# Kernel optimization log

Measured on AMD Instinct MI355X. Metric: run time of the kernel, lower is better.

## Reference

```python
import jax, jax.numpy as jnp
import numpy as np

B, TT, TS, H, O = 16, 512, 512, 1024, 1024


def setup_inputs() -> dict:
    key = jax.random.key(0)
    k1, k2, k3, k4, k5 = jax.random.split(key, 5)
    ht = jax.random.normal(k1, (B, TT, H), dtype=jnp.float32)
    hs = jax.random.normal(k2, (B, TS, H), dtype=jnp.float32)
    source = jax.random.randint(k3, (B, TS), 0, 10000, dtype=jnp.int32)
    # glorot-like scaling for weights
    W_a = jax.random.normal(k4, (H, H), dtype=jnp.float32) * (2.0 / (H + H)) ** 0.5
    W_c = jax.random.normal(k5, (2 * H, O), dtype=jnp.float32) * (2.0 / (2 * H + O)) ** 0.5
    b = jnp.zeros((O,), dtype=jnp.float32)
    return {"ht": ht, "hs": hs, "source": source, "W_a": W_a, "W_c": W_c, "b": b}


def reference(ht, hs, source, W_a, W_c, b):
    # score = ht . (hs @ W_a)^T : [B, Tt, Ts]
    keys = jnp.einsum('bsk,kl->bsl', hs, W_a)
    score = jnp.einsum('btk,bsk->bts', ht, keys)
    # stable exp with max subtraction (matches original manual softmax)
    score = jnp.exp(score - jnp.max(score, axis=-1, keepdims=True))
    # sequence mask from count of non-pad (non-zero) source tokens
    lens = jnp.sum((source != 0).astype(jnp.int32), axis=1)          # [B]
    mask = (jnp.arange(TS)[None, :] < lens[:, None]).astype(score.dtype)  # [B, Ts]
    score = score * mask[:, None, :]
    a = score / jnp.sum(score, axis=-1, keepdims=True)               # [B, Tt, Ts]
    c = jnp.einsum('bts,bsk->btk', a, hs)                            # context [B, Tt, H]
    h = jnp.concatenate([c, ht], axis=-1)                            # [B, Tt, 2H]
    return jnp.tanh(jnp.einsum('btk,kl->btl', h, W_c) + b)
```

## Files before the change

kernel.cpp:

```cpp
#include <hip/hip_runtime.h>
#include <math.h>

typedef unsigned short u16;
typedef unsigned int u32;

using f32x4 = __attribute__((ext_vector_type(4))) float;
using s16x8 = __attribute__((ext_vector_type(8))) short;
using f16x8 = __attribute__((ext_vector_type(8))) _Float16;
using u32x4 = __attribute__((ext_vector_type(4))) u32;

#define DEVI static __device__ __forceinline__

#define BB 16
#define TT 512
#define TS 512
#define HH 1024
#define OO 1024

DEVI void split_bf(float x, u16& hb, u16& lb) {
    u32 xb = __float_as_uint(x);
    float hf = __uint_as_float(xb & 0xffff0000u);
    hb = (u16)(xb >> 16);
    lb = (u16)(__float_as_uint(x - hf) >> 16);
}

DEVI float ub(u16 h) { return __uint_as_float((u32)h << 16); }

template <int PREC> struct FragT;
template <> struct FragT<0> { using T = s16x8; };
template <> struct FragT<1> { using T = f16x8; };

DEVI f32x4 mfma16(s16x8 a, s16x8 b, f32x4 c) {
    return __builtin_amdgcn_mfma_f32_16x16x32_bf16(a, b, c, 0, 0, 0);
}
DEVI f32x4 mfma16(f16x8 a, f16x8 b, f32x4 c) {
    return __builtin_amdgcn_mfma_f32_16x16x32_f16(a, b, c, 0, 0, 0);
}

DEVI void gl16(const void* g, void* l) {
    __builtin_amdgcn_global_load_lds(
        (__attribute__((address_space(1))) const void*)g,
        (__attribute__((address_space(3))) void*)l, 16, 0, 0);
}

__global__ void lens_kernel(const int* __restrict__ src, int* __restrict__ lens) {
    int b = blockIdx.x;
    int v = (src[b * TS + (int)threadIdx.x] != 0) ? 1 : 0;
    unsigned long long m = __ballot(v);
    __shared__ int part[8];
    if ((threadIdx.x & 63) == 0) part[threadIdx.x >> 6] = __popcll(m);
    __syncthreads();
    if (threadIdx.x == 0) {
        int s = 0;
#pragma unroll
        for (int i = 0; i < 8; ++i) s += part[i];
        lens[b] = s;
    }
}

template <int PREC>
__global__ void transpose_split_kernel(const float* __restrict__ src,
                                       u16* __restrict__ dhi, u16* __restrict__ dlo,
                                       int R, int C) {
    __shared__ float tile[32][33];
    long boff = (long)blockIdx.z * R * C;
    src += boff;
    dhi += boff;
    if (PREC == 0) dlo += boff;
    int c0 = blockIdx.x * 32, r0 = blockIdx.y * 32;
    int tx = threadIdx.x, ty = threadIdx.y;
#pragma unroll
    for (int i = 0; i < 32; i += 8)
        tile[ty + i][tx] = src[(long)(r0 + ty + i) * C + (c0 + tx)];
    __syncthreads();
#pragma unroll
    for (int i = 0; i < 32; i += 8) {
        float v = tile[tx][ty + i];
        long o = (long)(c0 + ty + i) * R + (r0 + tx);
        if constexpr (PREC == 0) {
            u16 hb, lb;
            split_bf(v, hb, lb);
            dhi[o] = hb;
            dlo[o] = lb;
        } else {
            dhi[o] = __builtin_bit_cast(u16, (_Float16)v);
        }
    }
}

__global__ void hs_prep_kernel(const float* __restrict__ src,
                               u16* __restrict__ rhi, u16* __restrict__ rlo,
                               u16* __restrict__ thi) {
    __shared__ float tile[32][33];
    long boff = (long)blockIdx.z * TS * HH;
    src += boff;
    rhi += boff;
    rlo += boff;
    thi += boff;
    int c0 = blockIdx.x * 32, r0 = blockIdx.y * 32;
    int tx = threadIdx.x, ty = threadIdx.y;
#pragma unroll
    for (int i = 0; i < 32; i += 8) {
        long o = (long)(r0 + ty + i) * HH + (c0 + tx);
        float v = src[o];
        tile[ty + i][tx] = v;
        u16 hb, lb;
        split_bf(v, hb, lb);
        rhi[o] = hb;
        rlo[o] = lb;
    }
    __syncthreads();
#pragma unroll
    for (int i = 0; i < 32; i += 8) {
        long o = (long)(c0 + ty + i) * TS + (r0 + tx);
        thi[o] = __builtin_bit_cast(u16, (_Float16)tile[tx][ty + i]);
    }
}

__global__ void htf_prep_kernel(const float* __restrict__ ht, u16* __restrict__ f) {
    long i = ((long)blockIdx.x * 256 + threadIdx.x) * 8;
    float4 v0 = *(const float4*)(ht + i);
    float4 v1 = *(const float4*)(ht + i + 4);
    float fv[8] = {v0.x, v0.y, v0.z, v0.w, v1.x, v1.y, v1.z, v1.w};
    f16x8 o;
#pragma unroll
    for (int j = 0; j < 8; ++j) o[j] = (_Float16)fv[j];
    *(f16x8*)(f + i) = o;
}

__global__ void softmax_mask_kernel(u16* __restrict__ h0, u16* __restrict__ l0,
                                    const u16* __restrict__ h1, const u16* __restrict__ l1,
                                    const int* __restrict__ lens) {
    long row = blockIdx.x;
    int len = lens[blockIdx.x >> 9];
    int lane = threadIdx.x;
    long o = row * TS + 8 * lane;
    s16x8 vh0 = *(const s16x8*)(h0 + o);
    s16x8 vl0 = *(const s16x8*)(l0 + o);
    s16x8 vh1 = *(const s16x8*)(h1 + o);
    s16x8 vl1 = *(const s16x8*)(l1 + o);
    float f[8];
#pragma unroll
    for (int i = 0; i < 8; ++i)
        f[i] = (ub((u16)vh0[i]) + ub((u16)vl0[i])) + (ub((u16)vh1[i]) + ub((u16)vl1[i]));
    float m = f[0];
#pragma unroll
    for (int i = 1; i < 8; ++i) m = fmaxf(m, f[i]);
#pragma unroll
    for (int os = 32; os > 0; os >>= 1) m = fmaxf(m, __shfl_xor(m, os));
    float e[8];
    float sum = 0.f;
#pragma unroll
    for (int i = 0; i < 8; ++i) {
        e[i] = (8 * lane + i < len) ? expf(f[i] - m) : 0.f;
        sum += e[i];
    }
#pragma unroll
    for (int os = 32; os > 0; os >>= 1) sum += __shfl_xor(sum, os);
    float inv = 1.0f / sum;
    f16x8 p;
#pragma unroll
    for (int i = 0; i < 8; ++i) p[i] = (_Float16)(e[i] * inv);
    *(f16x8*)(h0 + o) = p;
}

template <int PREC, int TERMS, int EPI, int ACON, int KSPLIT, int SWZ>
__global__ __launch_bounds__(512, 2)
void gemm_p(const u16* __restrict__ Ahi, const u16* __restrict__ Alo,
            const u16* __restrict__ A2,
            const u16* __restrict__ Bhi, const u16* __restrict__ Blo,
            float* __restrict__ C, u16* __restrict__ Chi, u16* __restrict__ Clo,
            const float* __restrict__ bias,
            int N, int K, int lda, int ldb,
            long sA, long sB, long sC, long sKh) {
    constexpr int SUBS = (TERMS == 3) ? 1 : 2;
    constexpr int BKI = 32 * SUBS;
    constexpr int SUBU = (TERMS == 3) ? 24576 : 12288;
    constexpr int BUFU = 24576;
    constexpr int AHo = 0;
    constexpr int ALof = 8192;
    constexpr int BHo = (TERMS == 3) ? 16384 : 8192;
    constexpr int BLof = 20480;

    __shared__ u16 lds[3 * BUFU];

    int bx, by, bz = 0;
    if (SWZ) {
        int id = blockIdx.x;
        int ns = ((id & 7) << 5) | (id >> 3);
        by = ns >> 3;
        bx = ns & 7;
    } else {
        bx = blockIdx.x;
        by = blockIdx.y;
        bz = blockIdx.z;
    }
    int kh = 0;
    if (KSPLIT == 2) {
        kh = bz & 1;
        bz >>= 1;
    }
    if (!ACON) {
        Ahi += (long)bz * sA + (long)kh * K;
        if (TERMS == 3) Alo += (long)bz * sA + (long)kh * K;
    }
    Bhi += (long)bz * sB + (long)kh * K;
    if (TERMS == 3) Blo += (long)bz * sB + (long)kh * K;

    int tid = threadIdx.x;
    int lane = tid & 63;
    int wave = tid >> 6;
    int wm = (wave >> 1) * 64;
    int wn = (wave & 1) * 64;
    int fr = lane & 15;
    int kq = lane >> 4;
    int m0 = by * 256;
    int n0 = bx * 128;

    f32x4 acc[4][4];
#pragma unroll
    for (int i = 0; i < 4; ++i)
#pragma unroll
        for (int j = 0; j < 4; ++j) acc[i][j] = (f32x4){0.f, 0.f, 0.f, 0.f};

    auto stage_arr = [&](int dst, const u16* g, int r0, int ldg, int k0, int cnt) {
#pragma unroll
        for (int h = 0; h < cnt; ++h) {
            int vt = tid + h * 512;
            int row = vt >> 2;
            int ls = (vt & 3) ^ ((row >> 1) & 3);
            const u16* gp = g + (long)(r0 + row) * ldg + (k0 + 8 * ls);
            u16* lp = lds + dst + ((tid & ~63) + h * 512) * 8;
            gl16(gp, lp);
        }
    };
    auto stage = [&](int bi, int t) {
#pragma unroll
        for (int s = 0; s < SUBS; ++s) {
            int ks = t * BKI + s * 32;
            int sb = bi * BUFU + s * ((TERMS == 3) ? 0 : SUBU);
            if (ACON) {
                if (ks < HH)
                    stage_arr(sb + AHo, Ahi, m0, lda, ks, 2);
                else
                    stage_arr(sb + AHo, A2, m0, lda, ks - HH, 2);
            } else {
                stage_arr(sb + AHo, Ahi, m0, lda, ks, 2);
                if (TERMS == 3) stage_arr(sb + ALof, Alo, m0, lda, ks, 2);
            }
            stage_arr(sb + BHo, Bhi, n0, ldb, ks, 1);
            if (TERMS == 3) stage_arr(sb + BLof, Blo, n0, ldb, ks, 1);
        }
    };

    const int NTI = K / BKI;
    stage(0, 0);
    stage(1, 1);
    stage(2, 2);
    asm volatile("s_waitcnt vmcnt(12)" ::: "memory");
    __builtin_amdgcn_sched_barrier(0);
    __builtin_amdgcn_s_barrier();
    __builtin_amdgcn_sched_barrier(0);

    using FT = typename FragT<PREC>::T;
    for (int t = 0; t < NTI; ++t) {
        if (t >= 1 && t + 2 < NTI) stage((t + 2) % 3, t + 2);

        const u16* Lb = lds + (t % 3) * BUFU;
#pragma unroll
        for (int s = 0; s < SUBS; ++s) {
            const u16* Ls = Lb + s * SUBU;
            FT afh[4], afl[4], bfh[4], bfl[4];
#pragma unroll
            for (int i = 0; i < 4; ++i) {
                int ra = wm + i * 16 + fr;
                int rb = wn + i * 16 + fr;
                int oa = ra * 32 + ((kq ^ ((ra >> 1) & 3)) << 3);
                int ob = rb * 32 + ((kq ^ ((rb >> 1) & 3)) << 3);
                afh[i] = *(const FT*)(Ls + AHo + oa);
                bfh[i] = *(const FT*)(Ls + BHo + ob);
                if (TERMS == 3) {
                    afl[i] = *(const FT*)(Ls + ALof + oa);
                    bfl[i] = *(const FT*)(Ls + BLof + ob);
                }
            }
            __builtin_amdgcn_s_setprio(1);
#pragma unroll
            for (int i = 0; i < 4; ++i)
#pragma unroll
                for (int j = 0; j < 4; ++j) {
                    acc[i][j] = mfma16(afh[i], bfh[j], acc[i][j]);
                    if (TERMS == 3) {
                        acc[i][j] = mfma16(afl[i], bfh[j], acc[i][j]);
                        acc[i][j] = mfma16(afh[i], bfl[j], acc[i][j]);
                    }
                }
            __builtin_amdgcn_s_setprio(0);
        }
        if (t < NTI - 1) {
            __builtin_amdgcn_sched_barrier(0);
            if (t + 2 < NTI)
                asm volatile("s_waitcnt vmcnt(6)" ::: "memory");
            else
                asm volatile("s_waitcnt vmcnt(0)" ::: "memory");
            __builtin_amdgcn_sched_barrier(0);
            __builtin_amdgcn_s_barrier();
            __builtin_amdgcn_sched_barrier(0);
        }
    }

    long obase = (long)bz * sC + (long)kh * sKh;
    int fq = (lane >> 4) * 4;
#pragma unroll
    for (int i = 0; i < 4; ++i)
#pragma unroll
        for (int j = 0; j < 4; ++j)
#pragma unroll
            for (int g = 0; g < 4; ++g) {
                int row = m0 + wm + i * 16 + fq + g;
                int col = n0 + wn + j * 16 + fr;
                long idx = obase + (long)row * N + col;
                float v = acc[i][j][g];
                if constexpr (EPI == 1) {
                    u16 h2, l2;
                    split_bf(v, h2, l2);
                    Chi[idx] = h2;
                    Clo[idx] = l2;
                } else if constexpr (EPI == 2) {
                    float x = v + bias[col];
                    float t2 = __expf(2.f * x);
                    C[idx] = 1.f - 2.f * __builtin_amdgcn_rcpf(t2 + 1.f);
                } else {
                    Chi[idx] = __builtin_bit_cast(u16, (_Float16)v);
                }
            }
}

template <int PREC, int ASRC, int EPI, int TERMS, int KSPLIT, bool SWZ>
__global__ __launch_bounds__(256, 2)
void gemm_u(const u16* __restrict__ Ahi, const u16* __restrict__ Alo,
            const float* __restrict__ Af,
            const u16* __restrict__ Bhi, const u16* __restrict__ Blo,
            float* __restrict__ C, u16* __restrict__ Chi, u16* __restrict__ Clo,
            const float* __restrict__ bias,
            int M, int N, int K, int lda, int ldb,
            long sA, long sB, long sC, long sKh) {
    int bx, by, bz;
    if (SWZ) {
        int id = blockIdx.x;
        int ns = ((id & 7) << 6) | (id >> 3);
        bx = ns & 7;
        by = ns >> 3;
        bz = 0;
    } else {
        bx = blockIdx.x;
        by = blockIdx.y;
        bz = blockIdx.z;
    }
    int kh = 0;
    if (KSPLIT == 2) {
        kh = bz & 1;
        bz >>= 1;
    }
    if (ASRC == 0) {
        Ahi += (long)bz * sA + (long)kh * K;
        if (TERMS == 3) Alo += (long)bz * sA + (long)kh * K;
    } else if (ASRC == 1) {
        Af += (long)bz * sA + (long)kh * K;
    }
    Bhi += (long)bz * sB + (long)kh * K;
    if (TERMS == 3) Blo += (long)bz * sB + (long)kh * K;

    int n0 = bx * 128;
    int m0 = by * 128;

    constexpr int NARR = (TERMS == 3) ? 4 : 2;
    constexpr int AH = 0, AL = 1;
    constexpr int BH = (TERMS == 3) ? 2 : 1;
    constexpr int BL = 3;
    __shared__ u16 lds[2][NARR * 4096];

    int tid = threadIdx.x;
    int lane = tid & 63;
    int wave = tid >> 6;
    int wm = (wave >> 1) * 64;
    int wn = (wave & 1) * 64;
    int fr = lane & 15;
    int kq = lane >> 4;

    f32x4 acc[4][4];
#pragma unroll
    for (int i = 0; i < 4; ++i)
#pragma unroll
        for (int j = 0; j < 4; ++j) acc[i][j] = (f32x4){0.f, 0.f, 0.f, 0.f};

    auto stage_gl = [&](int bufi, int arr, const u16* g, int r0, int ldg, int k0) {
#pragma unroll
        for (int h = 0; h < 2; ++h) {
            int vt = tid + h * 256;
            int row = vt >> 2;
            int ls = (vt & 3) ^ ((row >> 1) & 3);
            const u16* gp = g + (long)(r0 + row) * ldg + (k0 + 8 * ls);
            u16* lp = &lds[bufi][arr * 4096 + (vt >> 6) * 512];
            gl16(gp, lp);
        }
    };

    auto stage_a_f32 = [&](int bufi, const float* g, int ldg, int kk) {
        int r = tid >> 1;
        int hf = (tid & 1) * 16;
        const float* p = g + (long)(m0 + r) * ldg + kk + hf;
        float4 a0 = *(const float4*)(p + 0);
        float4 a1 = *(const float4*)(p + 4);
        float4 a2 = *(const float4*)(p + 8);
        float4 a3 = *(const float4*)(p + 12);
        float fv[16] = {a0.x, a0.y, a0.z, a0.w, a1.x, a1.y, a1.z, a1.w,
                        a2.x, a2.y, a2.z, a2.w, a3.x, a3.y, a3.z, a3.w};
        u16 hb[16], lb[16];
#pragma unroll
        for (int i = 0; i < 16; ++i) {
            if constexpr (PREC == 0)
                split_bf(fv[i], hb[i], lb[i]);
            else
                hb[i] = __builtin_bit_cast(u16, (_Float16)fv[i]);
        }
        int sw = (r >> 1) & 3;
        int ls0 = hf >> 3;
        u32x4 h0 = {(u32)hb[0] | ((u32)hb[1] << 16), (u32)hb[2] | ((u32)hb[3] << 16),
                    (u32)hb[4] | ((u32)hb[5] << 16), (u32)hb[6] | ((u32)hb[7] << 16)};
        u32x4 h1 = {(u32)hb[8] | ((u32)hb[9] << 16), (u32)hb[10] | ((u32)hb[11] << 16),
                    (u32)hb[12] | ((u32)hb[13] << 16), (u32)hb[14] | ((u32)hb[15] << 16)};
        u16* ah = &lds[bufi][AH * 4096 + r * 32];
        *(u32x4*)(ah + (((ls0 + 0) ^ sw) << 3)) = h0;
        *(u32x4*)(ah + (((ls0 + 1) ^ sw) << 3)) = h1;
        if constexpr (TERMS == 3) {
            u32x4 l0 = {(u32)lb[0] | ((u32)lb[1] << 16), (u32)lb[2] | ((u32)lb[3] << 16),
                        (u32)lb[4] | ((u32)lb[5] << 16), (u32)lb[6] | ((u32)lb[7] << 16)};
            u32x4 l1 = {(u32)lb[8] | ((u32)lb[9] << 16), (u32)lb[10] | ((u32)lb[11] << 16),
                        (u32)lb[12] | ((u32)lb[13] << 16), (u32)lb[14] | ((u32)lb[15] << 16)};
            u16* al = &lds[bufi][AL * 4096 + r * 32];
            *(u32x4*)(al + (((ls0 + 0) ^ sw) << 3)) = l0;
            *(u32x4*)(al + (((ls0 + 1) ^ sw) << 3)) = l1;
        }
    };

    auto stage = [&](int bufi, int t) {
        int k0 = t * 32;
        stage_gl(bufi, BH, Bhi, n0, ldb, k0);
        if (TERMS == 3) stage_gl(bufi, BL, Blo, n0, ldb, k0);
        if (ASRC == 0) {
            stage_gl(bufi, AH, Ahi, m0, lda, k0);
            if (TERMS == 3) stage_gl(bufi, AL, Alo, m0, lda, k0);
        } else {
            stage_a_f32(bufi, Af, lda, k0);
        }
    };

    const int NT = K / 32;
    stage(0, 0);
    __syncthreads();
    int cur = 0;
    using FT = typename FragT<PREC>::T;
    for (int t = 0; t < NT; ++t) {
        if (t + 1 < NT) stage(cur ^ 1, t + 1);

        const u16* L = lds[cur];
        FT afh[4], afl[4], bfh[4], bfl[4];
#pragma unroll
        for (int i = 0; i < 4; ++i) {
            int ra = wm + i * 16 + fr;
            int rb = wn + i * 16 + fr;
            int oa = ra * 32 + ((kq ^ ((ra >> 1) & 3)) << 3);
            int ob = rb * 32 + ((kq ^ ((rb >> 1) & 3)) << 3);
            afh[i] = *(const FT*)(L + AH * 4096 + oa);
            bfh[i] = *(const FT*)(L + BH * 4096 + ob);
            if (TERMS == 3) {
                afl[i] = *(const FT*)(L + AL * 4096 + oa);
                bfl[i] = *(const FT*)(L + BL * 4096 + ob);
            }
        }
#pragma unroll
        for (int i = 0; i < 4; ++i)
#pragma unroll
            for (int j = 0; j < 4; ++j) {
                acc[i][j] = mfma16(afh[i], bfh[j], acc[i][j]);
                if (TERMS == 3) {
                    acc[i][j] = mfma16(afl[i], bfh[j], acc[i][j]);
                    acc[i][j] = mfma16(afh[i], bfl[j], acc[i][j]);
                }
            }
        __syncthreads();
        cur ^= 1;
    }

    long obase = (long)bz * sC + (long)kh * sKh;
    int fq = (lane >> 4) * 4;
#pragma unroll
    for (int i = 0; i < 4; ++i)
#pragma unroll
        for (int j = 0; j < 4; ++j)
#pragma unroll
            for (int g = 0; g < 4; ++g) {
                int row = m0 + wm + i * 16 + fq + g;
                int col = n0 + wn + j * 16 + fr;
                long idx = obase + (long)row * N + col;
                float v = acc[i][j][g];
                if constexpr (EPI == 1) {
                    u16 h2, l2;
                    split_bf(v, h2, l2);
                    Chi[idx] = h2;
                    Clo[idx] = l2;
                } else if constexpr (EPI == 2) {
                    float x = v + bias[col];
                    float t2 = __expf(2.f * x);
                    C[idx] = 1.f - 2.f * __builtin_amdgcn_rcpf(t2 + 1.f);
                } else {
                    Chi[idx] = __builtin_bit_cast(u16, (_Float16)v);
                }
            }
}

extern "C" void kernel_launch(void* const* d_in, const int* in_sizes, int n_in,
                              void* d_out, int out_size, void* d_ws, size_t ws_size,
                              hipStream_t stream) {
    const float* ht = (const float*)d_in[0];
    const float* hs = (const float*)d_in[1];
    const int* source = (const int*)d_in[2];
    const float* Wa = (const float*)d_in[3];
    const float* Wc = (const float*)d_in[4];
    const float* bias = (const float*)d_in[5];
    float* out = (float*)d_out;

    char* w = (char*)d_ws;
    size_t off = 0;
    auto alloc = [&](size_t bytes) -> void* {
        void* p = w + off;
        off += (bytes + 255) & ~(size_t)255;
        return p;
    };
    int* lens = (int*)alloc(256);
    u16* keysHi = (u16*)alloc((size_t)BB * TS * HH * 2);
    u16* keysLo = (u16*)alloc((size_t)BB * TS * HH * 2);
    u16* hsRHi = (u16*)alloc((size_t)BB * TS * HH * 2);
    u16* hsRLo = (u16*)alloc((size_t)BB * TS * HH * 2);
    u16* hsTHi = (u16*)alloc((size_t)BB * HH * TS * 2);
    u16* WaTHi = (u16*)alloc((size_t)HH * HH * 2);
    u16* WaTLo = (u16*)alloc((size_t)HH * HH * 2);
    u16* scoreH0 = hsRHi;
    u16* scoreH1 = hsRHi + (size_t)BB * TT * TS;
    u16* scoreL0 = hsRLo;
    u16* scoreL1 = hsRLo + (size_t)BB * TT * TS;
    u16* cHi = keysHi;
    u16* WcTHi = scoreL0;
    u16* htF = hsTHi;
    u16* prob = scoreH0;

    lens_kernel<<<BB, TS, 0, stream>>>(source, lens);
    transpose_split_kernel<0><<<dim3(HH / 32, HH / 32, 1), dim3(32, 8), 0, stream>>>(
        Wa, WaTHi, WaTLo, HH, HH);
    hs_prep_kernel<<<dim3(HH / 32, TS / 32, BB), dim3(32, 8), 0, stream>>>(
        hs, hsRHi, hsRLo, hsTHi);

    gemm_p<0, 3, 1, 0, 1, 1><<<256, 512, 0, stream>>>(
        hsRHi, hsRLo, nullptr, WaTHi, WaTLo,
        nullptr, keysHi, keysLo, nullptr,
        HH, HH, HH, HH, 0, 0, 0, 0);

    gemm_u<0, 1, 1, 3, 2, false><<<dim3(TS / 128, TT / 128, 2 * BB), 256, 0, stream>>>(
        nullptr, nullptr, ht, keysHi, keysLo,
        nullptr, scoreH0, scoreL0, nullptr,
        TT, TS, HH / 2, HH, HH,
        (long)TT * HH, (long)TS * HH, (long)TT * TS, (long)BB * TT * TS);

    softmax_mask_kernel<<<BB * TT, 64, 0, stream>>>(scoreH0, scoreL0, scoreH1, scoreL1, lens);

    gemm_p<1, 1, 3, 0, 1, 0><<<dim3(8, 2, BB), 512, 0, stream>>>(
        prob, nullptr, nullptr, hsTHi, nullptr,
        nullptr, cHi, nullptr, nullptr,
        HH, TS, TS, TS,
        (long)TT * TS, (long)HH * TS, (long)TT * HH, 0);

    htf_prep_kernel<<<(BB * TT * HH) / (256 * 8), 256, 0, stream>>>(ht, htF);
    transpose_split_kernel<1><<<dim3(OO / 32, 2 * HH / 32, 1), dim3(32, 8), 0, stream>>>(
        Wc, WcTHi, nullptr, 2 * HH, OO);

    gemm_p<1, 1, 2, 1, 1, 1><<<256, 512, 0, stream>>>(
        cHi, nullptr, htF, WcTHi, nullptr,
        out, nullptr, nullptr, bias,
        OO, 2 * HH, HH, 2 * HH, 0, 0, 0, 0);
}
```

Before: 197.4 us.

## Interleave global-to-LDS prefetch chunks with MFMA phases in gemm_p main loop

```diff
diff --git a/kernel.cpp b/kernel.cpp
--- a/kernel.cpp
+++ b/kernel.cpp
@@ -42,6 +42,10 @@
         (__attribute__((address_space(1))) const void*)g,
         (__attribute__((address_space(3))) void*)l, 16, 0, 0);
 }
+
+#define SBAR() __builtin_amdgcn_sched_barrier(0)
+#define HBAR() __builtin_amdgcn_s_barrier()
+#define LGKM0() asm volatile("s_waitcnt lgkmcnt(0)" ::: "memory")
 
 __global__ void lens_kernel(const int* __restrict__ src, int* __restrict__ lens) {
     int b = blockIdx.x;
@@ -164,7 +168,7 @@
     *(f16x8*)(h0 + o) = p;
 }
 
-template <int PREC, int TERMS, int EPI, int ACON, int KSPLIT, int SWZ>
+template <int PREC, int TERMS, int EPI, int ACON, int SWZ>
 __global__ __launch_bounds__(512, 2)
 void gemm_p(const u16* __restrict__ Ahi, const u16* __restrict__ Alo,
             const u16* __restrict__ A2,
@@ -172,7 +176,7 @@
             float* __restrict__ C, u16* __restrict__ Chi, u16* __restrict__ Clo,
             const float* __restrict__ bias,
             int N, int K, int lda, int ldb,
-            long sA, long sB, long sC, long sKh) {
+            long sA, long sB, long sC) {
     constexpr int SUBS = (TERMS == 3) ? 1 : 2;
     constexpr int BKI = 32 * SUBS;
     constexpr int SUBU = (TERMS == 3) ? 24576 : 12288;
@@ -195,17 +199,12 @@
         by = blockIdx.y;
         bz = blockIdx.z;
     }
-    int kh = 0;
-    if (KSPLIT == 2) {
-        kh = bz & 1;
-        bz >>= 1;
-    }
     if (!ACON) {
-        Ahi += (long)bz * sA + (long)kh * K;
-        if (TERMS == 3) Alo += (long)bz * sA + (long)kh * K;
-    }
-    Bhi += (long)bz * sB + (long)kh * K;
-    if (TERMS == 3) Blo += (long)bz * sB + (long)kh * K;
+        Ahi += (long)bz * sA;
+        if (TERMS == 3) Alo += (long)bz * sA;
+    }
+    Bhi += (long)bz * sB;
+    if (TERMS == 3) Blo += (long)bz * sB;
 
     int tid = threadIdx.x;
     int lane = tid & 63;
@@ -234,11 +233,18 @@
             gl16(gp, lp);
         }
     };
-    auto stage = [&](int bi, int t) {
-#pragma unroll
-        for (int s = 0; s < SUBS; ++s) {
+    auto stage_part = [&](int bi, int t, int p) {
+        if constexpr (TERMS == 3) {
+            int ks = t * BKI;
+            int sb = bi * BUFU;
+            if (p == 0) stage_arr(sb + AHo, Ahi, m0, lda, ks, 2);
+            else if (p == 1) stage_arr(sb + ALof, Alo, m0, lda, ks, 2);
+            else if (p == 2) stage_arr(sb + BHo, Bhi, n0, ldb, ks, 1);
+            else stage_arr(sb + BLof, Blo, n0, ldb, ks, 1);
+        } else {
+            int s = p;
             int ks = t * BKI + s * 32;
-            int sb = bi * BUFU + s * ((TERMS == 3) ? 0 : SUBU);
+            int sb = bi * BUFU + s * SUBU;
             if (ACON) {
                 if (ks < HH)
                     stage_arr(sb + AHo, Ahi, m0, lda, ks, 2);
@@ -246,11 +252,27 @@
                     stage_arr(sb + AHo, A2, m0, lda, ks - HH, 2);
             } else {
                 stage_arr(sb + AHo, Ahi, m0, lda, ks, 2);
-                if (TERMS == 3) stage_arr(sb + ALof, Alo, m0, lda, ks, 2);
             }
             stage_arr(sb + BHo, Bhi, n0, ldb, ks, 1);
-            if (TERMS == 3) stage_arr(sb + BLof, Blo, n0, ldb, ks, 1);
-        }
+        }
+    };
+    auto stage = [&](int bi, int t) {
+#pragma unroll
+        for (int p = 0; p < ((TERMS == 3) ? 4 : 2); ++p) stage_part(bi, t, p);
+    };
+
+    using FT = typename FragT<PREC>::T;
+    auto rdA = [&](const u16* Ls, int i, FT& h, FT& l) {
+        int ra = wm + i * 16 + fr;
+        int oa = ra * 32 + ((kq ^ ((ra >> 1) & 3)) << 3);
+        h = *(const FT*)(Ls + AHo + oa);
+        if (TERMS == 3) l = *(const FT*)(Ls + ALof + oa);
+    };
+    auto rdB = [&](const u16* Ls, int j, FT& h, FT& l) {
+        int rb = wn + j * 16 + fr;
+        int ob = rb * 32 + ((kq ^ ((rb >> 1) & 3)) << 3);
+        h = *(const FT*)(Ls + BHo + ob);
+        if (TERMS == 3) l = *(const FT*)(Ls + BLof + ob);
     };
 
     const int NTI = K / BKI;
@@ -258,58 +280,86 @@
     stage(1, 1);
     stage(2, 2);
     asm volatile("s_waitcnt vmcnt(12)" ::: "memory");
-    __builtin_amdgcn_sched_barrier(0);
-    __builtin_amdgcn_s_barrier();
-    __builtin_amdgcn_sched_barrier(0);
-
-    using FT = typename FragT<PREC>::T;
+    SBAR();
+    HBAR();
+    SBAR();
+
     for (int t = 0; t < NTI; ++t) {
-        if (t >= 1 && t + 2 < NTI) stage((t + 2) % 3, t + 2);
-
         const u16* Lb = lds + (t % 3) * BUFU;
-#pragma unroll
-        for (int s = 0; s < SUBS; ++s) {
-            const u16* Ls = Lb + s * SUBU;
+        bool st = (t + 2 < NTI);
+        int b2 = (t + 2) % 3;
+        int t2 = t + 2;
+
+        if constexpr (TERMS == 3) {
             FT afh[4], afl[4], bfh[4], bfl[4];
 #pragma unroll
-            for (int i = 0; i < 4; ++i) {
-                int ra = wm + i * 16 + fr;
-                int rb = wn + i * 16 + fr;
-                int oa = ra * 32 + ((kq ^ ((ra >> 1) & 3)) << 3);
-                int ob = rb * 32 + ((kq ^ ((rb >> 1) & 3)) << 3);
-                afh[i] = *(const FT*)(Ls + AHo + oa);
-                bfh[i] = *(const FT*)(Ls + BHo + ob);
-                if (TERMS == 3) {
-                    afl[i] = *(const FT*)(Ls + ALof + oa);
-                    bfl[i] = *(const FT*)(Ls + BLof + ob);
+            for (int j = 0; j < 4; ++j) rdB(Lb, j, bfh[j], bfl[j]);
+            rdA(Lb, 0, afh[0], afl[0]);
+            if (st) stage_part(b2, t2, 0);
+            SBAR(); HBAR(); LGKM0(); SBAR();
+            __builtin_amdgcn_s_setprio(1);
+#pragma unroll
+            for (int j = 0; j < 4; ++j) {
+                acc[0][j] = mfma16(afh[0], bfh[j], acc[0][j]);
+                acc[0][j] = mfma16(afl[0], bfh[j], acc[0][j]);
+                acc[0][j] = mfma16(afh[0], bfl[j], acc[0][j]);
+            }
+            __builtin_amdgcn_s_setprio(0);
+            SBAR(); HBAR(); SBAR();
+#pragma unroll
+            for (int p = 1; p < 4; ++p) {
+                rdA(Lb, p, afh[p], afl[p]);
+                if (st) stage_part(b2, t2, p);
+                SBAR(); HBAR(); LGKM0(); SBAR();
+                __builtin_amdgcn_s_setprio(1);
+#pragma unroll
+                for (int j = 0; j < 4; ++j) {
+                    acc[p][j] = mfma16(afh[p], bfh[j], acc[p][j]);
+                    acc[p][j] = mfma16(afl[p], bfh[j], acc[p][j]);
+                    acc[p][j] = mfma16(afh[p], bfl[j], acc[p][j]);
                 }
-            }
-            __builtin_amdgcn_s_setprio(1);
-#pragma unroll
-            for (int i = 0; i < 4; ++i)
-#pragma unroll
-                for (int j = 0; j < 4; ++j) {
-                    acc[i][j] = mfma16(afh[i], bfh[j], acc[i][j]);
-                    if (TERMS == 3) {
-                        acc[i][j] = mfma16(afl[i], bfh[j], acc[i][j]);
-                        acc[i][j] = mfma16(afh[i], bfl[j], acc[i][j]);
-                    }
+                __builtin_amdgcn_s_setprio(0);
+                if (p < 3) {
+                    SBAR(); HBAR(); SBAR();
                 }
-            __builtin_amdgcn_s_setprio(0);
+            }
+        } else {
+#pragma unroll
+            for (int s = 0; s < 2; ++s) {
+                const u16* Ls = Lb + s * SUBU;
+                FT afh[4], afl[4], bfh[4], bfl[4];
+#pragma unroll
+                for (int i = 0; i < 4; ++i) {
+                    rdA(Ls, i, afh[i], afl[i]);
+                    rdB(Ls, i, bfh[i], bfl[i]);
+                }
+                if (st) stage_part(b2, t2, s);
+                SBAR(); HBAR(); LGKM0(); SBAR();
+                __builtin_amdgcn_s_setprio(1);
+#pragma unroll
+                for (int i = 0; i < 4; ++i)
+#pragma unroll
+                    for (int j = 0; j < 4; ++j)
+                        acc[i][j] = mfma16(afh[i], bfh[j], acc[i][j]);
+                __builtin_amdgcn_s_setprio(0);
+                if (s == 0) {
+                    SBAR(); HBAR(); SBAR();
+                }
+            }
         }
         if (t < NTI - 1) {
-            __builtin_amdgcn_sched_barrier(0);
-            if (t + 2 < NTI)
+            SBAR();
+            if (st)
                 asm volatile("s_waitcnt vmcnt(6)" ::: "memory");
             else
                 asm volatile("s_waitcnt vmcnt(0)" ::: "memory");
-            __builtin_amdgcn_sched_barrier(0);
-            __builtin_amdgcn_s_barrier();
-            __builtin_amdgcn_sched_barrier(0);
-        }
-    }
-
-    long obase = (long)bz * sC + (long)kh * sKh;
+            SBAR();
+            HBAR();
+            SBAR();
+        }
+    }
+
+    long obase = (long)bz * sC;
     int fq = (lane >> 4) * 4;
 #pragma unroll
     for (int i = 0; i < 4; ++i)
@@ -328,8 +378,8 @@
                     Clo[idx] = l2;
                 } else if constexpr (EPI == 2) {
                     float x = v + bias[col];
-                    float t2 = __expf(2.f * x);
-                    C[idx] = 1.f - 2.f * __builtin_amdgcn_rcpf(t2 + 1.f);
+                    float t2f = __expf(2.f * x);
+                    C[idx] = 1.f - 2.f * __builtin_amdgcn_rcpf(t2f + 1.f);
                 } else {
                     Chi[idx] = __builtin_bit_cast(u16, (_Float16)v);
                 }
@@ -561,10 +611,10 @@
     hs_prep_kernel<<<dim3(HH / 32, TS / 32, BB), dim3(32, 8), 0, stream>>>(
         hs, hsRHi, hsRLo, hsTHi);
 
-    gemm_p<0, 3, 1, 0, 1, 1><<<256, 512, 0, stream>>>(
+    gemm_p<0, 3, 1, 0, 1><<<256, 512, 0, stream>>>(
         hsRHi, hsRLo, nullptr, WaTHi, WaTLo,
         nullptr, keysHi, keysLo, nullptr,
-        HH, HH, HH, HH, 0, 0, 0, 0);
+        HH, HH, HH, HH, 0, 0, 0);
 
     gemm_u<0, 1, 1, 3, 2, false><<<dim3(TS / 128, TT / 128, 2 * BB), 256, 0, stream>>>(
         nullptr, nullptr, ht, keysHi, keysLo,
@@ -574,18 +624,18 @@
 
     softmax_mask_kernel<<<BB * TT, 64, 0, stream>>>(scoreH0, scoreL0, scoreH1, scoreL1, lens);
 
-    gemm_p<1, 1, 3, 0, 1, 0><<<dim3(8, 2, BB), 512, 0, stream>>>(
+    gemm_p<1, 1, 3, 0, 0><<<dim3(8, 2, BB), 512, 0, stream>>>(
         prob, nullptr, nullptr, hsTHi, nullptr,
         nullptr, cHi, nullptr, nullptr,
         HH, TS, TS, TS,
-        (long)TT * TS, (long)HH * TS, (long)TT * HH, 0);
+        (long)TT * TS, (long)HH * TS, (long)TT * HH);
 
     htf_prep_kernel<<<(BB * TT * HH) / (256 * 8), 256, 0, stream>>>(ht, htF);
     transpose_split_kernel<1><<<dim3(OO / 32, 2 * HH / 32, 1), dim3(32, 8), 0, stream>>>(
         Wc, WcTHi, nullptr, 2 * HH, OO);
 
-    gemm_p<1, 1, 2, 1, 1, 1><<<256, 512, 0, stream>>>(
+    gemm_p<1, 1, 2, 1, 1><<<256, 512, 0, stream>>>(
         cHi, nullptr, htF, WcTHi, nullptr,
         out, nullptr, nullptr, bias,
-        OO, 2 * HH, HH, 2 * HH, 0, 0, 0, 0);
-}
+        OO, 2 * HH, HH, 2 * HH, 0, 0, 0);
+}
```

Result: slower. 202.8 us (+2.7%).
